# Optimization experiments

Hardware: AMD Instinct MI355X
Metric: run time of the kernel (lower is better)

The kernel has to match this reference:

```python
import jax, jax.numpy as jnp
import numpy as np

INP = 64   # inplanes
PLN = 64   # planes
LOC = 64   # loc_planes
EPS = 1e-5


def _linear_init(key, fan_in, fan_out):
    # torch nn.Linear default: U(-1/sqrt(fan_in), 1/sqrt(fan_in)) for W and b
    kw, kb = jax.random.split(key)
    bound = 1.0 / np.sqrt(fan_in)
    W = jax.random.uniform(kw, (fan_in, fan_out), jnp.float32, -bound, bound)
    b = jax.random.uniform(kb, (fan_out,), jnp.float32, -bound, bound)
    return W, b


def setup_inputs() -> dict:
    key = jax.random.key(0)
    ks = jax.random.split(key, 8)
    B, N = 8, 4096
    img_fea = jax.random.normal(ks[0], (B, N, INP), jnp.float32)
    loc_fea = jax.random.normal(ks[1], (B, N, LOC), jnp.float32)
    W11, b11 = _linear_init(ks[2], INP + LOC, INP)
    W12, b12 = _linear_init(ks[3], INP, INP)
    W21, b21 = _linear_init(ks[4], INP + LOC, INP)
    W22, b22 = _linear_init(ks[5], INP, INP * PLN)
    W3, b3 = _linear_init(ks[6], PLN, PLN)
    ln_g = jnp.ones((PLN,), jnp.float32)
    ln_b = jnp.zeros((PLN,), jnp.float32)
    return {
        "img_fea": img_fea, "loc_fea": loc_fea,
        "W11": W11, "b11": b11, "W12": W12, "b12": b12,
        "W21": W21, "b21": b21, "W22": W22, "b22": b22,
        "ln_g": ln_g, "ln_b": ln_b, "W3": W3, "b3": b3,
    }


def reference(img_fea, loc_fea, W11, b11, W12, b12, W21, b21, W22, b22,
              ln_g, ln_b, W3, b3):
    B, N, C = img_fea.shape
    cat_fea = jnp.concatenate([img_fea, loc_fea], axis=2)  # [B,N,INP+LOC]
    # branch 1: per-token input vector
    w11 = jax.nn.relu(cat_fea @ W11 + b11)                 # [B,N,INP]
    w12 = w11 @ W12 + b12                                  # [B,N,INP]
    # branch 2: per-token weight matrix generation
    w21 = jax.nn.relu(cat_fea @ W21 + b21)                 # [B,N,INP]
    w22 = (w21 @ W22 + b22).reshape(B, N, INP, PLN)        # [B,N,INP,PLN]
    # batched tiny matvec: (1,INP) @ (INP,PLN) per token
    x = jnp.einsum('bni,bnio->bno', w12, w22)              # [B,N,PLN]
    # LayerNorm over last dim + ReLU
    mu = jnp.mean(x, axis=-1, keepdims=True)
    var = jnp.mean(jnp.square(x - mu), axis=-1, keepdims=True)
    x = (x - mu) * jax.lax.rsqrt(var + EPS) * ln_g + ln_b
    x = jax.nn.relu(x)
    # final linear (no activation)
    return x @ W3 + b3
```

## Files before the change

### kernel.cpp

```cpp
#include <hip/hip_runtime.h>
#include <cstdint>


typedef __bf16 bf16x4 __attribute__((ext_vector_type(4)));
typedef __bf16 bf16x8 __attribute__((ext_vector_type(8)));
typedef float  f32x4  __attribute__((ext_vector_type(4)));

#define MFMA16(A, B, C) __builtin_amdgcn_mfma_f32_16x16x32_bf16(A, B, C, 0, 0, 0)

#define SYNC_PIPE(N) asm volatile("s_waitcnt vmcnt(" #N ")\n\ts_barrier" ::: "memory")

#define OFF_BT22 0
#define OFF_W11  266240
#define OFF_W21  274432
#define OFF_W12  282624
#define OFF_W3   286720

__global__ __launch_bounds__(256) void prep_kernel(
    const float* __restrict__ W22, const float* __restrict__ b22,
    const float* __restrict__ W11, const float* __restrict__ W21,
    const float* __restrict__ W12, const float* __restrict__ W3,
    __bf16* __restrict__ ws)
{
    __shared__ __bf16 T[64][72];
    const int b = blockIdx.x, tid = threadIdx.x;
    const float* src; __bf16* dst;
    if (b < 64)       { src = W22 + b * 4096;        dst = ws + OFF_BT22 + b * 4096; }
    else if (b == 64) { src = b22;                   dst = ws + OFF_BT22 + 64 * 4096; }
    else if (b < 67)  { src = W11 + (b - 65) * 4096; dst = ws + OFF_W11 + (b - 65) * 4096; }
    else if (b < 69)  { src = W21 + (b - 67) * 4096; dst = ws + OFF_W21 + (b - 67) * 4096; }
    else if (b == 69) { src = W12;                   dst = ws + OFF_W12; }
    else              { src = W3;                    dst = ws + OFF_W3; }
    #pragma unroll
    for (int it = 0; it < 4; ++it) {
        int u = it * 1024 + tid * 4;
        int r = u >> 6, c = u & 63;
        const float4 v = *(const float4*)(src + u);
        T[r][c] = (__bf16)v.x; T[r][c + 1] = (__bf16)v.y;
        T[r][c + 2] = (__bf16)v.z; T[r][c + 3] = (__bf16)v.w;
    }
    __syncthreads();
    #pragma unroll
    for (int it = 0; it < 2; ++it) {
        int item = it * 256 + tid;
        int q = item >> 6, o = item & 63;
        bf16x8 pk;
        #pragma unroll
        for (int kj = 0; kj < 8; ++kj) pk[kj] = T[q * 8 + kj][o];
        *(bf16x8*)(dst + q * 512 + o * 8) = pk;
    }
}

__global__ __launch_bounds__(256, 2) void main_kernel(
    const float* __restrict__ img, const float* __restrict__ loc,
    const float* __restrict__ b11, const float* __restrict__ b12,
    const float* __restrict__ b21, const float* __restrict__ ln_g,
    const float* __restrict__ ln_b, const float* __restrict__ b3,
    const __bf16* __restrict__ ws, float* __restrict__ out)
{
    __shared__ __align__(1024) char smem[77824];
    __bf16* catL = (__bf16*)smem;
    __bf16* w11L = (__bf16*)(smem + 49152);
    __bf16* w21T = (__bf16*)(smem + 58368);
    __bf16* w12L = (__bf16*)(smem + 67584);
    float2* ps   = (float2*)(smem + 76800);

    const int tid  = threadIdx.x;
    const int wv   = tid >> 6;
    const int lane = tid & 63;
    const int ln   = lane & 15;
    const int quad = lane >> 4;
    const int th   = wv & 1;
    const int oh   = wv >> 1;
    const int wt   = th * 32;
    const int ob   = oh * 32;
    const long tb  = (long)blockIdx.x * 64;

    const __bf16* Bt22  = ws + OFF_BT22;
    const __bf16* W11bt = ws + OFF_W11;
    const __bf16* W21bt = ws + OFF_W21;
    const __bf16* W12bt = ws + OFF_W12;
    const __bf16* W3bt  = ws + OFF_W3;

    {
        const float* srcs[2] = {img, loc};
        #pragma unroll
        for (int s = 0; s < 2; ++s) {
            const float* src = srcs[s] + tb * 64;
            #pragma unroll
            for (int it = 0; it < 4; ++it) {
                int u = (it * 256 + tid) * 4;
                int t = u >> 6, c = u & 63;
                const float4 v = *(const float4*)(src + u);
                bf16x4 pk = {(__bf16)v.x, (__bf16)v.y, (__bf16)v.z, (__bf16)v.w};
                *(bf16x4*)(catL + t * 136 + s * 64 + c) = pk;
            }
        }
    }
    __syncthreads();

    {
        const __bf16* Wbt = oh ? W21bt : W11bt;
        const float* bsel = oh ? b21 : b11;
        f32x4 a1[2][4] = {};
        #pragma unroll
        for (int kb = 0; kb < 4; ++kb) {
            bf16x8 af[2];
            #pragma unroll
            for (int mf = 0; mf < 2; ++mf)
                af[mf] = *(const bf16x8*)(catL + (wt + mf*16 + ln)*136 + kb*32 + quad*8);
            #pragma unroll
            for (int nf = 0; nf < 4; ++nf) {
                bf16x8 bw = *(const bf16x8*)(Wbt + ((kb*4 + quad)*64 + nf*16 + ln)*8);
                #pragma unroll
                for (int mf = 0; mf < 2; ++mf)
                    a1[mf][nf] = MFMA16(af[mf], bw, a1[mf][nf]);
            }
        }
        if (oh == 0) {
            #pragma unroll
            for (int nf = 0; nf < 4; ++nf) {
                int o = nf*16 + ln;
                float cb = bsel[o];
                #pragma unroll
                for (int mf = 0; mf < 2; ++mf)
                    #pragma unroll
                    for (int r = 0; r < 4; ++r) {
                        int t = wt + mf*16 + quad*4 + r;
                        float v = a1[mf][nf][r] + cb; v = v > 0.f ? v : 0.f;
                        w11L[t*72 + o] = (__bf16)v;
                    }
            }
        } else {
            #pragma unroll
            for (int nf = 0; nf < 4; ++nf) {
                int o = nf*16 + ln;
                float cb = bsel[o];
                #pragma unroll
                for (int mf = 0; mf < 2; ++mf) {
                    bf16x4 pk;
                    #pragma unroll
                    for (int r = 0; r < 4; ++r) {
                        float v = a1[mf][nf][r] + cb; v = v > 0.f ? v : 0.f;
                        pk[r] = (__bf16)v;
                    }
                    *(bf16x4*)(w21T + o*72 + wt + mf*16 + quad*4) = pk;
                }
            }
        }
    }
    __syncthreads();

    float c12v[2];
    #pragma unroll
    for (int nf = 0; nf < 2; ++nf) c12v[nf] = b12[ob + nf*16 + ln];

    auto stage = [&](int c) {
        const int ng = (c == 32) ? 8 : 16;
        char* buf = smem + (c % 3) * 16384;
        for (int g = wv; g < ng; g += 4) {
            const __bf16* gsrc = Bt22 + ((long)c * 8192 + g * 512) + lane * 8;
            void* ldst = buf + g * 1024;
            __builtin_amdgcn_global_load_lds(
                (const __attribute__((address_space(1))) uint32_t*)gsrc,
                (__attribute__((address_space(3))) uint32_t*)ldst, 16, 0, 0);
        }
    };
    stage(0); stage(1);

    {
        f32x4 a12c[2][2] = {};
        #pragma unroll
        for (int kb = 0; kb < 2; ++kb) {
            bf16x8 af[2];
            #pragma unroll
            for (int mf = 0; mf < 2; ++mf)
                af[mf] = *(const bf16x8*)(w11L + (wt + mf*16 + ln)*72 + kb*32 + quad*8);
            #pragma unroll
            for (int nf = 0; nf < 2; ++nf) {
                bf16x8 bw = *(const bf16x8*)(W12bt + ((kb*4 + quad)*64 + ob + nf*16 + ln)*8);
                #pragma unroll
                for (int mf = 0; mf < 2; ++mf)
                    a12c[mf][nf] = MFMA16(af[mf], bw, a12c[mf][nf]);
            }
        }
        #pragma unroll
        for (int nf = 0; nf < 2; ++nf) {
            int o = ob + nf*16 + ln;
            #pragma unroll
            for (int mf = 0; mf < 2; ++mf)
                #pragma unroll
                for (int r = 0; r < 4; ++r) {
                    int t = wt + mf*16 + quad*4 + r;
                    w12L[t*72 + o] = (__bf16)(a12c[mf][nf][r] + c12v[nf]);
                }
        }
    }
    asm volatile("s_waitcnt vmcnt(4) lgkmcnt(0)\n\ts_barrier" ::: "memory");

    bf16x8 a12[2][2];
    #pragma unroll
    for (int mf = 0; mf < 2; ++mf)
        #pragma unroll
        for (int sub = 0; sub < 2; ++sub)
            a12[mf][sub] = *(const bf16x8*)(w12L + (wt + mf*16 + ln)*72 + sub*32 + quad*8);

    f32x4 acc[2][2] = {};
    for (int c = 0; c <= 32; ++c) {
        if (c <= 30) stage(c + 2);
        const __bf16* buf = (const __bf16*)(smem + (c % 3) * 16384);
        if (c < 32) {
            #pragma unroll
            for (int jj = 0; jj < 2; ++jj) {
                const int j = c*2 + jj;
                f32x4 w4[2];
                #pragma unroll
                for (int mf = 0; mf < 2; ++mf) {
                    bf16x4 wv4 = *(const bf16x4*)(w21T + j*72 + wt + mf*16 + quad*4);
                    w4[mf] = __builtin_convertvector(wv4, f32x4);
                }
                #pragma unroll
                for (int nf = 0; nf < 2; ++nf) {
                    bf16x8 bf0 = *(const bf16x8*)(buf + (jj*8     + quad)*512 + (ob + nf*16 + ln)*8);
                    bf16x8 bf1 = *(const bf16x8*)(buf + (jj*8 + 4 + quad)*512 + (ob + nf*16 + ln)*8);
                    #pragma unroll
                    for (int mf = 0; mf < 2; ++mf) {
                        f32x4 fz = {};
                        f32x4 m = MFMA16(a12[mf][0], bf0, fz);
                        m = MFMA16(a12[mf][1], bf1, m);
                        #pragma unroll
                        for (int r = 0; r < 4; ++r)
                            acc[mf][nf][r] = fmaf(w4[mf][r], m[r], acc[mf][nf][r]);
                    }
                }
            }
        } else {
            #pragma unroll
            for (int sub = 0; sub < 2; ++sub)
                #pragma unroll
                for (int nf = 0; nf < 2; ++nf) {
                    bf16x8 bfr = *(const bf16x8*)(buf + (sub*4 + quad)*512 + (ob + nf*16 + ln)*8);
                    #pragma unroll
                    for (int mf = 0; mf < 2; ++mf)
                        acc[mf][nf] = MFMA16(a12[mf][sub], bfr, acc[mf][nf]);
                }
        }
        if (c <= 29)      SYNC_PIPE(4);
        else if (c == 30) SYNC_PIPE(2);
        else if (c == 31) SYNC_PIPE(0);
    }

    #pragma unroll
    for (int mf = 0; mf < 2; ++mf)
        #pragma unroll
        for (int r = 0; r < 4; ++r) {
            float s1 = 0.f, s2 = 0.f;
            #pragma unroll
            for (int nf = 0; nf < 2; ++nf) { float v = acc[mf][nf][r]; s1 += v; s2 += v*v; }
            #pragma unroll
            for (int d = 1; d < 16; d <<= 1) {
                s1 += __shfl_xor(s1, d, 64);
                s2 += __shfl_xor(s2, d, 64);
            }
            if (ln == 0) {
                int t = wt + mf*16 + quad*4 + r;
                ps[t*2 + oh] = make_float2(s1, s2);
            }
        }
    __syncthreads();

    float gv[2], bv[2], b3v[2];
    #pragma unroll
    for (int nf = 0; nf < 2; ++nf) {
        int o = ob + nf*16 + ln;
        gv[nf] = ln_g[o]; bv[nf] = ln_b[o]; b3v[nf] = b3[o];
    }
    __bf16* xL = w12L;
    #pragma unroll
    for (int mf = 0; mf < 2; ++mf)
        #pragma unroll
        for (int r = 0; r < 4; ++r) {
            int t = wt + mf*16 + quad*4 + r;
            float2 p0 = ps[t*2], p1 = ps[t*2 + 1];
            float mean = (p0.x + p1.x) * 0.015625f;
            float var  = (p0.y + p1.y) * 0.015625f - mean * mean;
            float inv  = rsqrtf(var + 1e-5f);
            #pragma unroll
            for (int nf = 0; nf < 2; ++nf) {
                float v = (acc[mf][nf][r] - mean) * inv * gv[nf] + bv[nf];
                v = v > 0.f ? v : 0.f;
                xL[t*72 + ob + nf*16 + ln] = (__bf16)v;
            }
        }
    __syncthreads();

    f32x4 a3[2][2] = {};
    #pragma unroll
    for (int kb = 0; kb < 2; ++kb) {
        bf16x8 af[2];
        #pragma unroll
        for (int mf = 0; mf < 2; ++mf)
            af[mf] = *(const bf16x8*)(xL + (wt + mf*16 + ln)*72 + kb*32 + quad*8);
        #pragma unroll
        for (int nf = 0; nf < 2; ++nf) {
            bf16x8 bfr = *(const bf16x8*)(W3bt + ((kb*4 + quad)*64 + ob + nf*16 + ln)*8);
            #pragma unroll
            for (int mf = 0; mf < 2; ++mf)
                a3[mf][nf] = MFMA16(af[mf], bfr, a3[mf][nf]);
        }
    }
    #pragma unroll
    for (int mf = 0; mf < 2; ++mf)
        #pragma unroll
        for (int nf = 0; nf < 2; ++nf)
            #pragma unroll
            for (int r = 0; r < 4; ++r) {
                long t = tb + wt + mf*16 + quad*4 + r;
                out[t*64 + ob + nf*16 + ln] = a3[mf][nf][r] + b3v[nf];
            }
}

extern "C" void kernel_launch(void* const* d_in, const int* in_sizes, int n_in,
                              void* d_out, int out_size, void* d_ws, size_t ws_size,
                              hipStream_t stream)
{
    const float* img  = (const float*)d_in[0];
    const float* loc  = (const float*)d_in[1];
    const float* W11  = (const float*)d_in[2];
    const float* b11  = (const float*)d_in[3];
    const float* W12  = (const float*)d_in[4];
    const float* b12  = (const float*)d_in[5];
    const float* W21  = (const float*)d_in[6];
    const float* b21  = (const float*)d_in[7];
    const float* W22  = (const float*)d_in[8];
    const float* b22  = (const float*)d_in[9];
    const float* ln_g = (const float*)d_in[10];
    const float* ln_b = (const float*)d_in[11];
    const float* W3   = (const float*)d_in[12];
    const float* b3   = (const float*)d_in[13];
    __bf16* ws = (__bf16*)d_ws;
    float*  o  = (float*)d_out;

    prep_kernel<<<71, 256, 0, stream>>>(W22, b22, W11, W21, W12, W3, ws);
    main_kernel<<<512, 256, 0, stream>>>(img, loc, b11, b12, b21, ln_g, ln_b, b3, ws, o);
}
```

Measured before the change: 126.3 us.

## Split waves by output columns over all 64 tokens and shrink LDS footprint

The main kernel's wave decomposition changes from a 2x2 split over tokens and output halves to each wave owning 16 output columns across all 64 tokens. Each Bt22 fragment loaded from LDS is now reused across four token fragments, which reduces per-wave LDS reads of the large generated-weight tile. The LDS layout is repacked to alias the staging buffers with early-phase arrays, cutting shared memory from about 76KB to about 56KB so more blocks can be resident. In exchange, the per-token w21 scale reads double per wave, the W12 stage gains an extra barrier, and the LayerNorm statistics now need a four-way partial reduction.

```diff
diff --git a/kernel.cpp b/kernel.cpp
--- a/kernel.cpp
+++ b/kernel.cpp
@@ -58,22 +58,20 @@
     const float* __restrict__ ln_b, const float* __restrict__ b3,
     const __bf16* __restrict__ ws, float* __restrict__ out)
 {
-    __shared__ __align__(1024) char smem[77824];
+    __shared__ __align__(1024) char smem[57856];
     __bf16* catL = (__bf16*)smem;
-    __bf16* w11L = (__bf16*)(smem + 49152);
-    __bf16* w21T = (__bf16*)(smem + 58368);
-    __bf16* w12L = (__bf16*)(smem + 67584);
-    float2* ps   = (float2*)(smem + 76800);
+    __bf16* w11L = (__bf16*)(smem + 17920);
+    __bf16* w12L = (__bf16*)(smem + 27648);
+    float2* ps   = (float2*)smem;
+    __bf16* xL   = (__bf16*)(smem + 4096);
+    __bf16* w21T = (__bf16*)(smem + 49152);
 
     const int tid  = threadIdx.x;
     const int wv   = tid >> 6;
     const int lane = tid & 63;
     const int ln   = lane & 15;
     const int quad = lane >> 4;
-    const int th   = wv & 1;
-    const int oh   = wv >> 1;
-    const int wt   = th * 32;
-    const int ob   = oh * 32;
+    const int ob   = wv * 16;
     const long tb  = (long)blockIdx.x * 64;
 
     const __bf16* Bt22  = ws + OFF_BT22;
@@ -100,60 +98,90 @@
     __syncthreads();
 
     {
-        const __bf16* Wbt = oh ? W21bt : W11bt;
-        const float* bsel = oh ? b21 : b11;
-        f32x4 a1[2][4] = {};
+        const int isW21 = wv >> 1;
+        const int cb0 = (wv & 1) * 32;
+        const __bf16* Wbt = isW21 ? W21bt : W11bt;
+        const float* bsel = isW21 ? b21 : b11;
+        f32x4 a1[4][2] = {};
         #pragma unroll
         for (int kb = 0; kb < 4; ++kb) {
-            bf16x8 af[2];
-            #pragma unroll
-            for (int mf = 0; mf < 2; ++mf)
-                af[mf] = *(const bf16x8*)(catL + (wt + mf*16 + ln)*136 + kb*32 + quad*8);
-            #pragma unroll
-            for (int nf = 0; nf < 4; ++nf) {
-                bf16x8 bw = *(const bf16x8*)(Wbt + ((kb*4 + quad)*64 + nf*16 + ln)*8);
-                #pragma unroll
-                for (int mf = 0; mf < 2; ++mf)
+            bf16x8 af[4];
+            #pragma unroll
+            for (int mf = 0; mf < 4; ++mf)
+                af[mf] = *(const bf16x8*)(catL + (mf*16 + ln)*136 + kb*32 + quad*8);
+            #pragma unroll
+            for (int nf = 0; nf < 2; ++nf) {
+                bf16x8 bw = *(const bf16x8*)(Wbt + ((kb*4 + quad)*64 + cb0 + nf*16 + ln)*8);
+                #pragma unroll
+                for (int mf = 0; mf < 4; ++mf)
                     a1[mf][nf] = MFMA16(af[mf], bw, a1[mf][nf]);
             }
         }
-        if (oh == 0) {
-            #pragma unroll
-            for (int nf = 0; nf < 4; ++nf) {
-                int o = nf*16 + ln;
+        if (!isW21) {
+            #pragma unroll
+            for (int nf = 0; nf < 2; ++nf) {
+                int o = cb0 + nf*16 + ln;
                 float cb = bsel[o];
                 #pragma unroll
-                for (int mf = 0; mf < 2; ++mf)
+                for (int mf = 0; mf < 4; ++mf)
                     #pragma unroll
                     for (int r = 0; r < 4; ++r) {
-                        int t = wt + mf*16 + quad*4 + r;
+                        int t = mf*16 + quad*4 + r;
                         float v = a1[mf][nf][r] + cb; v = v > 0.f ? v : 0.f;
                         w11L[t*72 + o] = (__bf16)v;
                     }
             }
         } else {
             #pragma unroll
-            for (int nf = 0; nf < 4; ++nf) {
-                int o = nf*16 + ln;
+            for (int nf = 0; nf < 2; ++nf) {
+                int o = cb0 + nf*16 + ln;
                 float cb = bsel[o];
                 #pragma unroll
-                for (int mf = 0; mf < 2; ++mf) {
+                for (int mf = 0; mf < 4; ++mf) {
                     bf16x4 pk;
                     #pragma unroll
                     for (int r = 0; r < 4; ++r) {
                         float v = a1[mf][nf][r] + cb; v = v > 0.f ? v : 0.f;
                         pk[r] = (__bf16)v;
                     }
-                    *(bf16x4*)(w21T + o*72 + wt + mf*16 + quad*4) = pk;
+                    *(bf16x4*)(w21T + o*68 + mf*16 + quad*4) = pk;
                 }
             }
         }
     }
     __syncthreads();
 
-    float c12v[2];
-    #pragma unroll
-    for (int nf = 0; nf < 2; ++nf) c12v[nf] = b12[ob + nf*16 + ln];
+    {
+        float c12 = b12[ob + ln];
+        f32x4 a12c[4] = {};
+        #pragma unroll
+        for (int kb = 0; kb < 2; ++kb) {
+            bf16x8 af[4];
+            #pragma unroll
+            for (int mf = 0; mf < 4; ++mf)
+                af[mf] = *(const bf16x8*)(w11L + (mf*16 + ln)*72 + kb*32 + quad*8);
+            bf16x8 bw = *(const bf16x8*)(W12bt + ((kb*4 + quad)*64 + ob + ln)*8);
+            #pragma unroll
+            for (int mf = 0; mf < 4; ++mf)
+                a12c[mf] = MFMA16(af[mf], bw, a12c[mf]);
+        }
+        #pragma unroll
+        for (int mf = 0; mf < 4; ++mf)
+            #pragma unroll
+            for (int r = 0; r < 4; ++r) {
+                int t = mf*16 + quad*4 + r;
+                w12L[t*72 + ob + ln] = (__bf16)(a12c[mf][r] + c12);
+            }
+    }
+    __syncthreads();
+
+    bf16x8 a12[4][2];
+    #pragma unroll
+    for (int mf = 0; mf < 4; ++mf)
+        #pragma unroll
+        for (int sub = 0; sub < 2; ++sub)
+            a12[mf][sub] = *(const bf16x8*)(w12L + (mf*16 + ln)*72 + sub*32 + quad*8);
+    __syncthreads();
 
     auto stage = [&](int c) {
         const int ng = (c == 32) ? 8 : 16;
@@ -167,45 +195,9 @@
         }
     };
     stage(0); stage(1);
-
-    {
-        f32x4 a12c[2][2] = {};
-        #pragma unroll
-        for (int kb = 0; kb < 2; ++kb) {
-            bf16x8 af[2];
-            #pragma unroll
-            for (int mf = 0; mf < 2; ++mf)
-                af[mf] = *(const bf16x8*)(w11L + (wt + mf*16 + ln)*72 + kb*32 + quad*8);
-            #pragma unroll
-            for (int nf = 0; nf < 2; ++nf) {
-                bf16x8 bw = *(const bf16x8*)(W12bt + ((kb*4 + quad)*64 + ob + nf*16 + ln)*8);
-                #pragma unroll
-                for (int mf = 0; mf < 2; ++mf)
-                    a12c[mf][nf] = MFMA16(af[mf], bw, a12c[mf][nf]);
-            }
-        }
-        #pragma unroll
-        for (int nf = 0; nf < 2; ++nf) {
-            int o = ob + nf*16 + ln;
-            #pragma unroll
-            for (int mf = 0; mf < 2; ++mf)
-                #pragma unroll
-                for (int r = 0; r < 4; ++r) {
-                    int t = wt + mf*16 + quad*4 + r;
-                    w12L[t*72 + o] = (__bf16)(a12c[mf][nf][r] + c12v[nf]);
-                }
-        }
-    }
-    asm volatile("s_waitcnt vmcnt(4) lgkmcnt(0)\n\ts_barrier" ::: "memory");
-
-    bf16x8 a12[2][2];
-    #pragma unroll
-    for (int mf = 0; mf < 2; ++mf)
-        #pragma unroll
-        for (int sub = 0; sub < 2; ++sub)
-            a12[mf][sub] = *(const bf16x8*)(w12L + (wt + mf*16 + ln)*72 + sub*32 + quad*8);
-
-    f32x4 acc[2][2] = {};
+    SYNC_PIPE(4);
+
+    f32x4 acc[4] = {};
     for (int c = 0; c <= 32; ++c) {
         if (c <= 30) stage(c + 2);
         const __bf16* buf = (const __bf16*)(smem + (c % 3) * 16384);
@@ -213,37 +205,32 @@
             #pragma unroll
             for (int jj = 0; jj < 2; ++jj) {
                 const int j = c*2 + jj;
-                f32x4 w4[2];
-                #pragma unroll
-                for (int mf = 0; mf < 2; ++mf) {
-                    bf16x4 wv4 = *(const bf16x4*)(w21T + j*72 + wt + mf*16 + quad*4);
+                f32x4 w4[4];
+                #pragma unroll
+                for (int mf = 0; mf < 4; ++mf) {
+                    bf16x4 wv4 = *(const bf16x4*)(w21T + j*68 + mf*16 + quad*4);
                     w4[mf] = __builtin_convertvector(wv4, f32x4);
                 }
-                #pragma unroll
-                for (int nf = 0; nf < 2; ++nf) {
-                    bf16x8 bf0 = *(const bf16x8*)(buf + (jj*8     + quad)*512 + (ob + nf*16 + ln)*8);
-                    bf16x8 bf1 = *(const bf16x8*)(buf + (jj*8 + 4 + quad)*512 + (ob + nf*16 + ln)*8);
+                bf16x8 bf0 = *(const bf16x8*)(buf + (jj*8     + quad)*512 + (ob + ln)*8);
+                bf16x8 bf1 = *(const bf16x8*)(buf + (jj*8 + 4 + quad)*512 + (ob + ln)*8);
+                #pragma unroll
+                for (int mf = 0; mf < 4; ++mf) {
+                    f32x4 fz = {};
+                    f32x4 m = MFMA16(a12[mf][0], bf0, fz);
+                    m = MFMA16(a12[mf][1], bf1, m);
                     #pragma unroll
-                    for (int mf = 0; mf < 2; ++mf) {
-                        f32x4 fz = {};
-                        f32x4 m = MFMA16(a12[mf][0], bf0, fz);
-                        m = MFMA16(a12[mf][1], bf1, m);
-                        #pragma unroll
-                        for (int r = 0; r < 4; ++r)
-                            acc[mf][nf][r] = fmaf(w4[mf][r], m[r], acc[mf][nf][r]);
-                    }
+                    for (int r = 0; r < 4; ++r)
+                        acc[mf][r] = fmaf(w4[mf][r], m[r], acc[mf][r]);
                 }
             }
         } else {
             #pragma unroll
-            for (int sub = 0; sub < 2; ++sub)
-                #pragma unroll
-                for (int nf = 0; nf < 2; ++nf) {
-                    bf16x8 bfr = *(const bf16x8*)(buf + (sub*4 + quad)*512 + (ob + nf*16 + ln)*8);
-                    #pragma unroll
-                    for (int mf = 0; mf < 2; ++mf)
-                        acc[mf][nf] = MFMA16(a12[mf][sub], bfr, acc[mf][nf]);
-                }
+            for (int sub = 0; sub < 2; ++sub) {
+                bf16x8 bfr = *(const bf16x8*)(buf + (sub*4 + quad)*512 + (ob + ln)*8);
+                #pragma unroll
+                for (int mf = 0; mf < 4; ++mf)
+                    acc[mf] = MFMA16(a12[mf][sub], bfr, acc[mf]);
+            }
         }
         if (c <= 29)      SYNC_PIPE(4);
         else if (c == 30) SYNC_PIPE(2);
@@ -251,73 +238,58 @@
     }
 
     #pragma unroll
-    for (int mf = 0; mf < 2; ++mf)
+    for (int mf = 0; mf < 4; ++mf)
         #pragma unroll
         for (int r = 0; r < 4; ++r) {
-            float s1 = 0.f, s2 = 0.f;
-            #pragma unroll
-            for (int nf = 0; nf < 2; ++nf) { float v = acc[mf][nf][r]; s1 += v; s2 += v*v; }
+            float v = acc[mf][r];
+            float s1 = v, s2 = v*v;
             #pragma unroll
             for (int d = 1; d < 16; d <<= 1) {
                 s1 += __shfl_xor(s1, d, 64);
                 s2 += __shfl_xor(s2, d, 64);
             }
             if (ln == 0) {
-                int t = wt + mf*16 + quad*4 + r;
-                ps[t*2 + oh] = make_float2(s1, s2);
-            }
-        }
-    __syncthreads();
-
-    float gv[2], bv[2], b3v[2];
-    #pragma unroll
-    for (int nf = 0; nf < 2; ++nf) {
-        int o = ob + nf*16 + ln;
-        gv[nf] = ln_g[o]; bv[nf] = ln_b[o]; b3v[nf] = b3[o];
-    }
-    __bf16* xL = w12L;
-    #pragma unroll
-    for (int mf = 0; mf < 2; ++mf)
+                int t = mf*16 + quad*4 + r;
+                ps[t*4 + wv] = make_float2(s1, s2);
+            }
+        }
+    __syncthreads();
+
+    float gv = ln_g[ob + ln], bv = ln_b[ob + ln], b3v = b3[ob + ln];
+    #pragma unroll
+    for (int mf = 0; mf < 4; ++mf)
         #pragma unroll
         for (int r = 0; r < 4; ++r) {
-            int t = wt + mf*16 + quad*4 + r;
-            float2 p0 = ps[t*2], p1 = ps[t*2 + 1];
-            float mean = (p0.x + p1.x) * 0.015625f;
-            float var  = (p0.y + p1.y) * 0.015625f - mean * mean;
+            int t = mf*16 + quad*4 + r;
+            float2 p0 = ps[t*4], p1 = ps[t*4 + 1], p2 = ps[t*4 + 2], p3 = ps[t*4 + 3];
+            float mean = (p0.x + p1.x + p2.x + p3.x) * 0.015625f;
+            float var  = (p0.y + p1.y + p2.y + p3.y) * 0.015625f - mean * mean;
             float inv  = rsqrtf(var + 1e-5f);
-            #pragma unroll
-            for (int nf = 0; nf < 2; ++nf) {
-                float v = (acc[mf][nf][r] - mean) * inv * gv[nf] + bv[nf];
-                v = v > 0.f ? v : 0.f;
-                xL[t*72 + ob + nf*16 + ln] = (__bf16)v;
-            }
-        }
-    __syncthreads();
-
-    f32x4 a3[2][2] = {};
+            float v = (acc[mf][r] - mean) * inv * gv + bv;
+            v = v > 0.f ? v : 0.f;
+            xL[t*72 + ob + ln] = (__bf16)v;
+        }
+    __syncthreads();
+
+    f32x4 a3[4] = {};
     #pragma unroll
     for (int kb = 0; kb < 2; ++kb) {
-        bf16x8 af[2];
-        #pragma unroll
-        for (int mf = 0; mf < 2; ++mf)
-            af[mf] = *(const bf16x8*)(xL + (wt + mf*16 + ln)*72 + kb*32 + quad*8);
-        #pragma unroll
-        for (int nf = 0; nf < 2; ++nf) {
-            bf16x8 bfr = *(const bf16x8*)(W3bt + ((kb*4 + quad)*64 + ob + nf*16 + ln)*8);
-            #pragma unroll
-            for (int mf = 0; mf < 2; ++mf)
-                a3[mf][nf] = MFMA16(af[mf], bfr, a3[mf][nf]);
-        }
-    }
-    #pragma unroll
-    for (int mf = 0; mf < 2; ++mf)
-        #pragma unroll
-        for (int nf = 0; nf < 2; ++nf)
-            #pragma unroll
-            for (int r = 0; r < 4; ++r) {
-                long t = tb + wt + mf*16 + quad*4 + r;
-                out[t*64 + ob + nf*16 + ln] = a3[mf][nf][r] + b3v[nf];
-            }
+        bf16x8 af[4];
+        #pragma unroll
+        for (int mf = 0; mf < 4; ++mf)
+            af[mf] = *(const bf16x8*)(xL + (mf*16 + ln)*72 + kb*32 + quad*8);
+        bf16x8 bfr = *(const bf16x8*)(W3bt + ((kb*4 + quad)*64 + ob + ln)*8);
+        #pragma unroll
+        for (int mf = 0; mf < 4; ++mf)
+            a3[mf] = MFMA16(af[mf], bfr, a3[mf]);
+    }
+    #pragma unroll
+    for (int mf = 0; mf < 4; ++mf)
+        #pragma unroll
+        for (int r = 0; r < 4; ++r) {
+            long t = tb + mf*16 + quad*4 + r;
+            out[t*64 + ob + ln] = a3[mf][r] + b3v;
+        }
 }
 
 extern "C" void kernel_launch(void* const* d_in, const int* in_sizes, int n_in,
```

New measurement: 127.7 us. No clear change (+1.1%).
